# Performance work log

Measured on AMD Instinct MI355X. Metric: run time of the kernel, lower is better.

The kernel has to match this reference:

```python
import jax, jax.numpy as jnp
import numpy as np

B, T, I, H, L, O = 2048, 512, 1, 64, 2, 1


def _lstm_layer(x, Wih, Whh, b):
    """Single LSTM layer, batch_first x: [B, T, in] -> [B, T, H].
    PyTorch gate order: i, f, g, o. b = b_ih + b_hh (folded)."""
    Bn = x.shape[0]
    Hn = Whh.shape[1]
    # Precompute input contribution for all timesteps (hoisted out of scan)
    xg = jnp.einsum('bti,gi->btg', x, Wih) + b  # [B, T, 4H]

    def step(carry, xg_t):
        h, c = carry
        g = xg_t + h @ Whh.T  # [B, 4H]
        i, f, gg, o = jnp.split(g, 4, axis=-1)
        i = jax.nn.sigmoid(i)
        f = jax.nn.sigmoid(f)
        gg = jnp.tanh(gg)
        o = jax.nn.sigmoid(o)
        c = f * c + i * gg
        h = o * jnp.tanh(c)
        return (h, c), h

    h0 = jnp.zeros((Bn, Hn), x.dtype)
    c0 = jnp.zeros((Bn, Hn), x.dtype)
    (_, _), hs = jax.lax.scan(step, (h0, c0), jnp.swapaxes(xg, 0, 1))  # hs: [T, B, H]
    return jnp.swapaxes(hs, 0, 1)


def setup_inputs() -> dict:
    key = jax.random.key(0)
    ks = jax.random.split(key, 11)
    s = 1.0 / np.sqrt(H)  # torch default uniform bound
    u = lambda k, shp: jax.random.uniform(k, shp, jnp.float32, -s, s)
    return {
        'x': jax.random.normal(ks[0], (B, T, I), jnp.float32),
        'Wih0': u(ks[1], (4 * H, I)),
        'Whh0': u(ks[2], (4 * H, H)),
        'bih0': u(ks[3], (4 * H,)),
        'bhh0': u(ks[4], (4 * H,)),
        'Wih1': u(ks[5], (4 * H, H)),
        'Whh1': u(ks[6], (4 * H, H)),
        'bih1': u(ks[7], (4 * H,)),
        'bhh1': u(ks[8], (4 * H,)),
        'fcW': u(ks[9], (O, H)),
        'fcb': u(ks[10], (O,)),
    }


def reference(x, Wih0, Whh0, bih0, bhh0, Wih1, Whh1, bih1, bhh1, fcW, fcb):
    h1 = _lstm_layer(x, Wih0, Whh0, bih0 + bhh0)   # [B, T, H]
    h2 = _lstm_layer(h1, Wih1, Whh1, bih1 + bhh1)  # [B, T, H]
    return h2[:, -1, :] @ fcW.T + fcb               # [B, O]
```

## Files before the change

### kernel.cpp

```cpp
#include <hip/hip_runtime.h>


#define TT 512
#define HH 64
#define BT 8

typedef __attribute__((ext_vector_type(4))) int i32x4;

#define MFMAI8 __builtin_amdgcn_mfma_i32_16x16x64_i8

#define WSCALE 260096.0f
#define HSCALE 32512.0f
constexpr float C_MID = (float)(256.0 / (260096.0 * 32512.0));

__device__ __forceinline__ float sigm(float x) {
    return __builtin_amdgcn_rcpf(1.f + __expf(-x));
}
__device__ __forceinline__ float tanh_f(float x) {
    return 1.f - 2.f * __builtin_amdgcn_rcpf(1.f + __expf(2.f * x));
}
__device__ __forceinline__ float gate4(float pi, float pf, float pg, float po, float& c) {
    float gi = sigm(pi), gf = sigm(pf), gg = tanh_f(pg), go = sigm(po);
    c = fmaf(gf, c, gi * gg);
    return go * tanh_f(c);
}
__device__ __forceinline__ float dpp_ror8(float v) {
    return __int_as_float(__builtin_amdgcn_update_dpp(
        0, __float_as_int(v), 0x128, 0xF, 0xF, true));
}
__device__ __forceinline__ void cvtW16(const float* __restrict__ p, i32x4& hi, i32x4& lo) {
    #pragma unroll
    for (int r = 0; r < 4; ++r) {
        int hw = 0, lw = 0;
        #pragma unroll
        for (int b = 0; b < 4; ++b) {
            int wq = (int)rintf(p[r * 4 + b] * WSCALE);
            int h8 = (wq + 128) >> 8;
            int l8 = wq - (h8 << 8);
            hw |= (h8 & 0xFF) << (8 * b);
            lw |= (l8 & 0xFF) << (8 * b);
        }
        hi[r] = hw; lo[r] = lw;
    }
}

__global__ __launch_bounds__(1024) void lstm_mfma(
    const float* __restrict__ x,
    const float* __restrict__ Wih0, const float* __restrict__ Whh0,
    const float* __restrict__ bih0, const float* __restrict__ bhh0,
    const float* __restrict__ Wih1, const float* __restrict__ Whh1,
    const float* __restrict__ bih1, const float* __restrict__ bhh1,
    const float* __restrict__ fcW, const float* __restrict__ fcb,
    float* __restrict__ out)
{
    __shared__ float xs[BT][TT + 1];
    __shared__ __align__(16) signed char aH[2][2][2][64][16];
    __shared__ float hF[BT][HH + 1];
    __shared__ float fcw_s[HH];

    const int t    = threadIdx.x;
    const int lane = t & 63;
    const int w    = t >> 6;
    const int b0   = blockIdx.x * BT;
    const int m    = lane & 15;
    const int q    = lane >> 4;
    const int ts   = m >> 3;
    const int bpk  = m & 7;
    const int jpk  = 4 * w + q;

    for (int i = t; i < BT * TT; i += 1024)
        xs[i >> 9][i & (TT - 1)] = x[(size_t)(b0 + (i >> 9)) * TT + (i & (TT - 1))];
    {
        int* z = (int*)aH;
        for (int i = t; i < 2048; i += 1024) z[i] = 0;
    }
    if (t < HH) fcw_s[t] = fcW[t];

    i32x4 A0h, A0l, I1h, I1l, H1h, H1l;
    {
        const int rho = (m & 3) * 64 + 4 * w + (m >> 2);
        cvtW16(Whh0 + rho * HH + q * 16, A0h, A0l);
        cvtW16(Wih1 + rho * HH + q * 16, I1h, I1l);
        cvtW16(Whh1 + rho * HH + q * 16, H1h, H1l);
    }

    float wxb[4], bia[4];
    #pragma unroll
    for (int v = 0; v < 4; ++v) {
        const int r = v * 64 + jpk;
        if (ts) { wxb[v] = 0.f;     bia[v] = bih1[r] + bhh1[r]; }
        else    { wxb[v] = Wih0[r]; bia[v] = bih0[r] + bhh0[r]; }
    }
    const int wl = ((jpk >> 4) << 4) + bpk;
    const int wb = jpk & 15;
    float c = 0.f;

    __syncthreads();

    #pragma unroll 2
    for (int k = 0; k < TT; ++k) {
        const int p = k & 1, pn = p ^ 1;
        i32x4 bh1 = *(const i32x4*)&aH[0][p][0][lane][0];
        i32x4 bl1 = *(const i32x4*)&aH[0][p][1][lane][0];
        i32x4 bh2 = *(const i32x4*)&aH[1][p][0][lane][0];
        i32x4 bl2 = *(const i32x4*)&aH[1][p][1][lane][0];
        i32x4 z4 = {0, 0, 0, 0};
        i32x4 aHHr = z4, aMDr = z4, bHHr = z4, bMDr = z4;
        aHHr = MFMAI8(A0h, bh1, aHHr, 0, 0, 0);
        bHHr = MFMAI8(I1h, bh1, bHHr, 0, 0, 0);
        aMDr = MFMAI8(A0h, bl1, aMDr, 0, 0, 0);
        bMDr = MFMAI8(I1h, bl1, bMDr, 0, 0, 0);
        aMDr = MFMAI8(A0l, bh1, aMDr, 0, 0, 0);
        bMDr = MFMAI8(I1l, bh1, bMDr, 0, 0, 0);
        bHHr = MFMAI8(H1h, bh2, bHHr, 0, 0, 0);
        bMDr = MFMAI8(H1h, bl2, bMDr, 0, 0, 0);
        bMDr = MFMAI8(H1l, bh2, bMDr, 0, 0, 0);

        float pk4[4];
        #pragma unroll
        for (int r = 0; r < 4; ++r) {
            float pa = (float)((aHHr[r] << 8) + aMDr[r]) * C_MID;
            float pb = (float)((bHHr[r] << 8) + bMDr[r]) * C_MID;
            float mv = dpp_ror8(pb);
            pk4[r] = (m < 8) ? pa : mv;
        }
        float xb = xs[bpk][k];
        float hv = gate4(pk4[0] + fmaf(wxb[0], xb, bia[0]),
                         pk4[1] + fmaf(wxb[1], xb, bia[1]),
                         pk4[2] + fmaf(wxb[2], xb, bia[2]),
                         pk4[3] + fmaf(wxb[3], xb, bia[3]), c);
        if (k == 0) {
            hv = ts ? 0.f : hv;
            c  = ts ? 0.f : c;
        }
        int hq = __float_as_int(fmaf(hv, HSCALE, 12582912.f)) - 0x4B400000;
        int h8 = (hq + 128) >> 8;
        int l8 = hq - (h8 << 8);
        aH[ts][pn][0][wl][wb] = (signed char)h8;
        aH[ts][pn][1][wl][wb] = (signed char)l8;
        __syncthreads();
    }

    {
        i32x4 bh1 = *(const i32x4*)&aH[0][0][0][lane][0];
        i32x4 bl1 = *(const i32x4*)&aH[0][0][1][lane][0];
        i32x4 bh2 = *(const i32x4*)&aH[1][0][0][lane][0];
        i32x4 bl2 = *(const i32x4*)&aH[1][0][1][lane][0];
        i32x4 z4 = {0, 0, 0, 0};
        i32x4 bHHr = z4, bMDr = z4;
        bHHr = MFMAI8(I1h, bh1, bHHr, 0, 0, 0);
        bMDr = MFMAI8(I1h, bl1, bMDr, 0, 0, 0);
        bMDr = MFMAI8(I1l, bh1, bMDr, 0, 0, 0);
        bHHr = MFMAI8(H1h, bh2, bHHr, 0, 0, 0);
        bMDr = MFMAI8(H1h, bl2, bMDr, 0, 0, 0);
        bMDr = MFMAI8(H1l, bh2, bMDr, 0, 0, 0);
        float pk4[4];
        #pragma unroll
        for (int r = 0; r < 4; ++r) {
            float pb = (float)((bHHr[r] << 8) + bMDr[r]) * C_MID;
            pk4[r] = dpp_ror8(pb);
        }
        float hv = gate4(pk4[0] + bia[0], pk4[1] + bia[1],
                         pk4[2] + bia[2], pk4[3] + bia[3], c);
        if (ts) hF[bpk][jpk] = hv;
    }
    __syncthreads();

    if (t < BT) {
        float s = fcb[0];
        #pragma unroll 8
        for (int j = 0; j < HH; ++j)
            s = fmaf(hF[t][j], fcw_s[j], s);
        out[b0 + t] = s;
    }
}

extern "C" void kernel_launch(void* const* d_in, const int* in_sizes, int n_in,
                              void* d_out, int out_size, void* d_ws, size_t ws_size,
                              hipStream_t stream) {
    const float* x    = (const float*)d_in[0];
    const float* Wih0 = (const float*)d_in[1];
    const float* Whh0 = (const float*)d_in[2];
    const float* bih0 = (const float*)d_in[3];
    const float* bhh0 = (const float*)d_in[4];
    const float* Wih1 = (const float*)d_in[5];
    const float* Whh1 = (const float*)d_in[6];
    const float* bih1 = (const float*)d_in[7];
    const float* bhh1 = (const float*)d_in[8];
    const float* fcW  = (const float*)d_in[9];
    const float* fcb  = (const float*)d_in[10];
    float* out = (float*)d_out;

    lstm_mfma<<<dim3(2048 / BT), dim3(1024), 0, stream>>>(
        x, Wih0, Whh0, bih0, bhh0, Wih1, Whh1, bih1, bhh1, fcW, fcb, out);
}
```

Before: 445.8 us.

## Fold exp scaling into constants, offset-encode low bytes, combine layers in integer domain

Folds the log2(e) and tanh factor-of-two scaling into the dequantisation constants and biases, so the gates can use the raw hardware exp2 instruction directly. The low byte of h is now stored offset by 128 instead of rounding split, with a precomputed weight-row-sum correction seeding the accumulators. Layer-0 and layer-1 results are merged with an integer DPP add before a single float conversion. The weight byte packing and h-store index are also permuted. This trims per-step ALU work on the serial critical path, at the cost of subtler quantisation bookkeeping that must stay exactly consistent.

Result: faster. 433.9 us (-2.7%).

```diff
diff --git a/kernel.cpp b/kernel.cpp
--- a/kernel.cpp
+++ b/kernel.cpp
@@ -11,22 +11,27 @@
 
 #define WSCALE 260096.0f
 #define HSCALE 32512.0f
-constexpr float C_MID = (float)(256.0 / (260096.0 * 32512.0));
-
-__device__ __forceinline__ float sigm(float x) {
-    return __builtin_amdgcn_rcpf(1.f + __expf(-x));
-}
-__device__ __forceinline__ float tanh_f(float x) {
-    return 1.f - 2.f * __builtin_amdgcn_rcpf(1.f + __expf(2.f * x));
-}
-__device__ __forceinline__ float gate4(float pi, float pf, float pg, float po, float& c) {
-    float gi = sigm(pi), gf = sigm(pf), gg = tanh_f(pg), go = sigm(po);
+#define LOG2E  1.44269504f
+constexpr float C_SIG = (float)(256.0 / (260096.0 * 32512.0) * 1.4426950408889634);
+constexpr float C_TGH = (float)(2.0 * 256.0 / (260096.0 * 32512.0) * 1.4426950408889634);
+
+__device__ __forceinline__ float exp2_hw(float x) {
+    float r; asm("v_exp_f32 %0, %1" : "=v"(r) : "v"(x)); return r;
+}
+__device__ __forceinline__ float exp2n_hw(float x) {
+    float r; asm("v_exp_f32 %0, -%1" : "=v"(r) : "v"(x)); return r;
+}
+__device__ __forceinline__ float gate4s(float p0, float p1, float p2, float p3, float& c) {
+    float gi = __builtin_amdgcn_rcpf(1.f + exp2n_hw(p0));
+    float gf = __builtin_amdgcn_rcpf(1.f + exp2n_hw(p1));
+    float gg = 1.f - 2.f * __builtin_amdgcn_rcpf(1.f + exp2_hw(p2));
+    float go = __builtin_amdgcn_rcpf(1.f + exp2n_hw(p3));
     c = fmaf(gf, c, gi * gg);
-    return go * tanh_f(c);
-}
-__device__ __forceinline__ float dpp_ror8(float v) {
-    return __int_as_float(__builtin_amdgcn_update_dpp(
-        0, __float_as_int(v), 0x128, 0xF, 0xF, true));
+    float tc = 1.f - 2.f * __builtin_amdgcn_rcpf(1.f + exp2_hw(c * (2.f * LOG2E)));
+    return go * tc;
+}
+__device__ __forceinline__ int dpp_ror8_i(int v) {
+    return __builtin_amdgcn_update_dpp(v, v, 0x128, 0xF, 0xF, true);
 }
 __device__ __forceinline__ void cvtW16(const float* __restrict__ p, i32x4& hi, i32x4& lo) {
     #pragma unroll
@@ -34,7 +39,7 @@
         int hw = 0, lw = 0;
         #pragma unroll
         for (int b = 0; b < 4; ++b) {
-            int wq = (int)rintf(p[r * 4 + b] * WSCALE);
+            int wq = (int)rintf(p[4 * b + r] * WSCALE);
             int h8 = (wq + 128) >> 8;
             int l8 = wq - (h8 << 8);
             hw |= (h8 & 0xFF) << (8 * b);
@@ -72,7 +77,8 @@
         xs[i >> 9][i & (TT - 1)] = x[(size_t)(b0 + (i >> 9)) * TT + (i & (TT - 1))];
     {
         int* z = (int*)aH;
-        for (int i = t; i < 2048; i += 1024) z[i] = 0;
+        for (int i = t; i < 2048; i += 1024)
+            z[i] = ((i >> 8) & 1) ? 0x80808080 : 0;
     }
     if (t < HH) fcw_s[t] = fcW[t];
 
@@ -84,15 +90,28 @@
         cvtW16(Whh1 + rho * HH + q * 16, H1h, H1l);
     }
 
+    i32x4 corrA, corrB;
+    {
+        i32x4 ones; ones[0] = 0x01010101; ones[1] = 0x01010101;
+        ones[2] = 0x01010101; ones[3] = 0x01010101;
+        i32x4 zz = {0, 0, 0, 0};
+        i32x4 Sa = MFMAI8(A0h, ones, zz, 0, 0, 0);
+        i32x4 Sb = MFMAI8(I1h, ones, zz, 0, 0, 0);
+        Sb = MFMAI8(H1h, ones, Sb, 0, 0, 0);
+        #pragma unroll
+        for (int r = 0; r < 4; ++r) { corrA[r] = Sa[r] << 7; corrB[r] = Sb[r] << 7; }
+    }
+
     float wxb[4], bia[4];
     #pragma unroll
     for (int v = 0; v < 4; ++v) {
         const int r = v * 64 + jpk;
-        if (ts) { wxb[v] = 0.f;     bia[v] = bih1[r] + bhh1[r]; }
-        else    { wxb[v] = Wih0[r]; bia[v] = bih0[r] + bhh0[r]; }
+        const float sc = (v == 2) ? 2.f * LOG2E : LOG2E;
+        if (ts) { wxb[v] = 0.f;          bia[v] = (bih1[r] + bhh1[r]) * sc; }
+        else    { wxb[v] = Wih0[r] * sc; bia[v] = (bih0[r] + bhh0[r]) * sc; }
     }
     const int wl = ((jpk >> 4) << 4) + bpk;
-    const int wb = jpk & 15;
+    const int wb = ((jpk & 3) << 2) | ((jpk >> 2) & 3);
     float c = 0.f;
 
     __syncthreads();
@@ -105,7 +124,8 @@
         i32x4 bh2 = *(const i32x4*)&aH[1][p][0][lane][0];
         i32x4 bl2 = *(const i32x4*)&aH[1][p][1][lane][0];
         i32x4 z4 = {0, 0, 0, 0};
-        i32x4 aHHr = z4, aMDr = z4, bHHr = z4, bMDr = z4;
+        i32x4 aHHr = z4, bHHr = z4;
+        i32x4 aMDr = corrA, bMDr = corrB;
         aHHr = MFMAI8(A0h, bh1, aHHr, 0, 0, 0);
         bHHr = MFMAI8(I1h, bh1, bHHr, 0, 0, 0);
         aMDr = MFMAI8(A0h, bl1, aMDr, 0, 0, 0);
@@ -116,28 +136,24 @@
         bMDr = MFMAI8(H1h, bl2, bMDr, 0, 0, 0);
         bMDr = MFMAI8(H1l, bh2, bMDr, 0, 0, 0);
 
-        float pk4[4];
+        float xb = xs[bpk][k];
+        float pre[4];
         #pragma unroll
         for (int r = 0; r < 4; ++r) {
-            float pa = (float)((aHHr[r] << 8) + aMDr[r]) * C_MID;
-            float pb = (float)((bHHr[r] << 8) + bMDr[r]) * C_MID;
-            float mv = dpp_ror8(pb);
-            pk4[r] = (m < 8) ? pa : mv;
-        }
-        float xb = xs[bpk][k];
-        float hv = gate4(pk4[0] + fmaf(wxb[0], xb, bia[0]),
-                         pk4[1] + fmaf(wxb[1], xb, bia[1]),
-                         pk4[2] + fmaf(wxb[2], xb, bia[2]),
-                         pk4[3] + fmaf(wxb[3], xb, bia[3]), c);
+            int hh = aHHr[r] + dpp_ror8_i(bHHr[r]);
+            int md = aMDr[r] + dpp_ror8_i(bMDr[r]);
+            float P = (float)((hh << 8) + md);
+            const float Cr = (r == 2) ? C_TGH : C_SIG;
+            pre[r] = fmaf(P, Cr, fmaf(wxb[r], xb, bia[r]));
+        }
+        float hv = gate4s(pre[0], pre[1], pre[2], pre[3], c);
         if (k == 0) {
             hv = ts ? 0.f : hv;
             c  = ts ? 0.f : c;
         }
         int hq = __float_as_int(fmaf(hv, HSCALE, 12582912.f)) - 0x4B400000;
-        int h8 = (hq + 128) >> 8;
-        int l8 = hq - (h8 << 8);
-        aH[ts][pn][0][wl][wb] = (signed char)h8;
-        aH[ts][pn][1][wl][wb] = (signed char)l8;
+        aH[ts][pn][0][wl][wb] = (signed char)(hq >> 8);
+        aH[ts][pn][1][wl][wb] = (signed char)(hq ^ 0x80);
         __syncthreads();
     }
 
@@ -147,21 +163,23 @@
         i32x4 bh2 = *(const i32x4*)&aH[1][0][0][lane][0];
         i32x4 bl2 = *(const i32x4*)&aH[1][0][1][lane][0];
         i32x4 z4 = {0, 0, 0, 0};
-        i32x4 bHHr = z4, bMDr = z4;
+        i32x4 bHHr = z4, bMDr = corrB;
         bHHr = MFMAI8(I1h, bh1, bHHr, 0, 0, 0);
         bMDr = MFMAI8(I1h, bl1, bMDr, 0, 0, 0);
         bMDr = MFMAI8(I1l, bh1, bMDr, 0, 0, 0);
         bHHr = MFMAI8(H1h, bh2, bHHr, 0, 0, 0);
         bMDr = MFMAI8(H1h, bl2, bMDr, 0, 0, 0);
         bMDr = MFMAI8(H1l, bh2, bMDr, 0, 0, 0);
-        float pk4[4];
+        float pre[4];
         #pragma unroll
         for (int r = 0; r < 4; ++r) {
-            float pb = (float)((bHHr[r] << 8) + bMDr[r]) * C_MID;
-            pk4[r] = dpp_ror8(pb);
-        }
-        float hv = gate4(pk4[0] + bia[0], pk4[1] + bia[1],
-                         pk4[2] + bia[2], pk4[3] + bia[3], c);
+            int hh = dpp_ror8_i(bHHr[r]);
+            int md = dpp_ror8_i(bMDr[r]);
+            float P = (float)((hh << 8) + md);
+            const float Cr = (r == 2) ? C_TGH : C_SIG;
+            pre[r] = fmaf(P, Cr, bia[r]);
+        }
+        float hv = gate4s(pre[0], pre[1], pre[2], pre[3], c);
         if (ts) hF[bpk][jpk] = hv;
     }
     __syncthreads();
```
